# Kernel optimization log

Hardware: AMD Instinct MI355X
Metric: run time of the kernel (lower is better)

## Reference

```python
import jax, jax.numpy as jnp
import numpy as np

UNITS = 512
CONN = 512          # input feature dim (connections)
DEND_SIZE = 16
SEQL = CONN // DEND_SIZE  # 32 dendrite segments per unit
BATCH = 512


def _make_dendrites(units, conn, dsize, seed=0):
    # Per-unit random permutation of input indices, grouped into contiguous
    # dendrites of size dsize -> segment id in [0, seql) for every input index.
    rng = np.random.default_rng(seed)
    seql = conn // dsize
    seg = np.empty((units, conn), dtype=np.int32)
    for u in range(units):
        perm = rng.permutation(conn)
        for s in range(seql):
            seg[u, perm[dsize * s:dsize * (s + 1)]] = s
    return seg


def setup_inputs() -> dict:
    key = jax.random.key(0)
    k1, k2, k3, k4 = jax.random.split(key, 4)
    x = jax.random.normal(k1, (BATCH, CONN), dtype=jnp.float32)
    # weight_twice & not uniqueW -> per-unit scalar input weight, shape [1, units]
    kernel = jax.random.uniform(k2, (1, UNITS), dtype=jnp.float32, minval=5e-5, maxval=0.1)
    # per-(segment, unit) dendritic weight, shape [seql, units]
    dendriticW = jax.random.uniform(k3, (SEQL, UNITS), dtype=jnp.float32, minval=5e-5, maxval=0.1)
    bias = jax.random.normal(k4, (UNITS,), dtype=jnp.float32) * 0.05
    dendrites = jnp.asarray(_make_dendrites(UNITS, CONN, DEND_SIZE))  # [units, conn] int32
    return {"x": x, "kernel": kernel, "dendriticW": dendriticW,
            "bias": bias, "dendrites": dendrites}


def reference(x, kernel, dendriticW, bias, dendrites):
    # x: [batch, conn]; dendrites: [units, conn] segment ids in [0, SEQL)
    xT = x.T  # [conn, batch]
    # per-unit gather + unsorted_segment_sum over connections -> [units, seql, batch]
    segsum = jax.vmap(lambda seg: jax.ops.segment_sum(xT, seg, num_segments=SEQL))(dendrites)
    # weight_twice: per-unit scalar input weight (kernel broadcast over conn)
    segsum = segsum * kernel[0][:, None, None]
    # dendritic weighting + reduction over segments -> [batch, units]
    out = jnp.einsum('usb,su->bu', segsum, dendriticW) + bias
    return jax.nn.relu(out)
```

## Files before the change

### kernel.cpp

```cpp
#include <hip/hip_runtime.h>
#include <hip/hip_bf16.h>

#define UNITS 512
#define CONN  512
#define SEQL  32

typedef __hip_bfloat16 bf16;
typedef __attribute__((ext_vector_type(8))) short short8;
typedef __attribute__((ext_vector_type(4))) float floatx4;


union cv8 { bf16 h[8]; short8 v; };

__device__ __forceinline__ short8 cvt8(const float* p) {
    const float4 f0 = ((const float4*)p)[0];
    const float4 f1 = ((const float4*)p)[1];
    cv8 a;
    a.h[0] = __float2bfloat16(f0.x); a.h[1] = __float2bfloat16(f0.y);
    a.h[2] = __float2bfloat16(f0.z); a.h[3] = __float2bfloat16(f0.w);
    a.h[4] = __float2bfloat16(f1.x); a.h[5] = __float2bfloat16(f1.y);
    a.h[6] = __float2bfloat16(f1.z); a.h[7] = __float2bfloat16(f1.w);
    return a.v;
}

__global__ __launch_bounds__(256) void dendriter_fused_v2(
    const float* __restrict__ x,
    const float* __restrict__ kern,
    const float* __restrict__ dW,
    const float* __restrict__ bias,
    const int*   __restrict__ dend,
    float* __restrict__ out)
{
    __shared__ float  table[16][SEQL];
    __shared__ short8 wl[16][65];

    const int t  = threadIdx.x;
    const int ut = blockIdx.x * 16;
    const int bt = blockIdx.y * 64;

    const int lane = t & 63;
    const int wv   = t >> 6;
    const int m    = lane & 15;
    const int q    = lane >> 4;
    const int btw  = bt + wv * 16;
    const float* xrow = x + (size_t)(btw + m) * CONN + q * 8;
    short8 afr[16];
#pragma unroll
    for (int kb = 0; kb < 16; ++kb)
        afr[kb] = cvt8(xrow + kb * 32);

#pragma unroll
    for (int e = t; e < 16 * SEQL; e += 256) {
        const int seg = e >> 4, ul = e & 15;
        table[ul][seg] = kern[ut + ul] * dW[seg * UNITS + ut + ul];
    }
    __syncthreads();

    {
        const int ul  = t >> 4;
        const int cg0 = (t & 15) * 4;
        const int4* dp = (const int4*)(dend + (size_t)(ut + ul) * CONN + cg0 * 8);
#pragma unroll
        for (int j = 0; j < 4; ++j) {
            const int4 s0 = dp[2 * j];
            const int4 s1 = dp[2 * j + 1];
            const int segs[8] = {s0.x, s0.y, s0.z, s0.w, s1.x, s1.y, s1.z, s1.w};
            cv8 w;
#pragma unroll
            for (int i = 0; i < 8; ++i)
                w.h[i] = __float2bfloat16(table[ul][segs[i]]);
            const int cg = cg0 + j;
            wl[cg >> 2][ul | ((cg & 3) << 4)] = w.v;
        }
    }
    __syncthreads();

    floatx4 acc = {0.f, 0.f, 0.f, 0.f};
#pragma unroll
    for (int kb = 0; kb < 16; ++kb)
        acc = __builtin_amdgcn_mfma_f32_16x16x32_bf16(afr[kb], wl[kb][lane],
                                                      acc, 0, 0, 0);

    const float bu = bias[ut + m];
#pragma unroll
    for (int r = 0; r < 4; ++r) {
        float v = acc[r] + bu;
        v = v > 0.f ? v : 0.f;
        out[(size_t)(btw + q * 4 + r) * UNITS + ut + m] = v;
    }
}

extern "C" void kernel_launch(void* const* d_in, const int* in_sizes, int n_in,
                              void* d_out, int out_size, void* d_ws, size_t ws_size,
                              hipStream_t stream) {
    const float* x    = (const float*)d_in[0];
    const float* kern = (const float*)d_in[1];
    const float* dW   = (const float*)d_in[2];
    const float* bias = (const float*)d_in[3];
    const int*   dend = (const int*)  d_in[4];
    float* out = (float*)d_out;

    const int batch = in_sizes[0] / CONN;
    (void)d_ws; (void)ws_size;

    dendriter_fused_v2<<<dim3(UNITS / 16, batch / 64), 256, 0, stream>>>(
        x, kern, dW, bias, dend, out);
}
```

Baseline: 67.13 us.

## Split K dimension across waves with LDS reduction and shrink batch tile

Each block now covers 16 batch rows instead of 64, and its four waves split the 512-wide reduction into quarters, combining partial MFMA accumulators through shared memory. This launches four times as many blocks to raise parallelism and cuts per-thread register use for the x fragments. Dendrite index loads are also issued early into registers so they overlap the table build. In exchange the weight table is rebuilt four times as often across the grid, and an extra barrier plus LDS reduction is added.

```diff
diff --git a/kernel.cpp b/kernel.cpp
--- a/kernel.cpp
+++ b/kernel.cpp
@@ -23,7 +23,7 @@
     return a.v;
 }
 
-__global__ __launch_bounds__(256) void dendriter_fused_v2(
+__global__ __launch_bounds__(256) void dendriter_v3(
     const float* __restrict__ x,
     const float* __restrict__ kern,
     const float* __restrict__ dW,
@@ -31,62 +31,71 @@
     const int*   __restrict__ dend,
     float* __restrict__ out)
 {
-    __shared__ float  table[16][SEQL];
-    __shared__ short8 wl[16][65];
+    __shared__ float   table[16][SEQL];
+    __shared__ short8  wl[16][65];
+    __shared__ floatx4 red[3][64];
 
-    const int t  = threadIdx.x;
-    const int ut = blockIdx.x * 16;
-    const int bt = blockIdx.y * 64;
-
+    const int t    = threadIdx.x;
+    const int ut   = blockIdx.x * 16;
+    const int bt   = blockIdx.y * 16;
     const int lane = t & 63;
     const int wv   = t >> 6;
     const int m    = lane & 15;
     const int q    = lane >> 4;
-    const int btw  = bt + wv * 16;
-    const float* xrow = x + (size_t)(btw + m) * CONN + q * 8;
-    short8 afr[16];
+
+    const float* xrow = x + (size_t)(bt + m) * CONN + q * 8;
+    short8 afr[4];
 #pragma unroll
-    for (int kb = 0; kb < 16; ++kb)
-        afr[kb] = cvt8(xrow + kb * 32);
+    for (int j = 0; j < 4; ++j)
+        afr[j] = cvt8(xrow + (wv * 4 + j) * 32);
+
+    const int ul  = t >> 4;
+    const int cg0 = (t & 15) * 4;
+    const int4* dp = (const int4*)(dend + (size_t)(ut + ul) * CONN + cg0 * 8);
+    int4 sreg[8];
+#pragma unroll
+    for (int j = 0; j < 8; ++j) sreg[j] = dp[j];
 
 #pragma unroll
     for (int e = t; e < 16 * SEQL; e += 256) {
-        const int seg = e >> 4, ul = e & 15;
-        table[ul][seg] = kern[ut + ul] * dW[seg * UNITS + ut + ul];
+        const int seg = e >> 4, uu = e & 15;
+        table[uu][seg] = kern[ut + uu] * dW[seg * UNITS + ut + uu];
     }
     __syncthreads();
 
-    {
-        const int ul  = t >> 4;
-        const int cg0 = (t & 15) * 4;
-        const int4* dp = (const int4*)(dend + (size_t)(ut + ul) * CONN + cg0 * 8);
 #pragma unroll
-        for (int j = 0; j < 4; ++j) {
-            const int4 s0 = dp[2 * j];
-            const int4 s1 = dp[2 * j + 1];
-            const int segs[8] = {s0.x, s0.y, s0.z, s0.w, s1.x, s1.y, s1.z, s1.w};
-            cv8 w;
+    for (int j = 0; j < 4; ++j) {
+        const int4 s0 = sreg[2 * j];
+        const int4 s1 = sreg[2 * j + 1];
+        const int segs[8] = {s0.x, s0.y, s0.z, s0.w, s1.x, s1.y, s1.z, s1.w};
+        cv8 w;
 #pragma unroll
-            for (int i = 0; i < 8; ++i)
-                w.h[i] = __float2bfloat16(table[ul][segs[i]]);
-            const int cg = cg0 + j;
-            wl[cg >> 2][ul | ((cg & 3) << 4)] = w.v;
-        }
+        for (int i = 0; i < 8; ++i)
+            w.h[i] = __float2bfloat16(table[ul][segs[i]]);
+        const int cg = cg0 + j;
+        wl[cg >> 2][ul | ((cg & 3) << 4)] = w.v;
     }
     __syncthreads();
 
     floatx4 acc = {0.f, 0.f, 0.f, 0.f};
 #pragma unroll
-    for (int kb = 0; kb < 16; ++kb)
-        acc = __builtin_amdgcn_mfma_f32_16x16x32_bf16(afr[kb], wl[kb][lane],
-                                                      acc, 0, 0, 0);
+    for (int j = 0; j < 4; ++j)
+        acc = __builtin_amdgcn_mfma_f32_16x16x32_bf16(afr[j],
+                  wl[wv * 4 + j][lane], acc, 0, 0, 0);
 
-    const float bu = bias[ut + m];
+    if (wv) red[wv - 1][lane] = acc;
+    __syncthreads();
+    if (wv == 0) {
+        acc += red[0][lane];
+        acc += red[1][lane];
+        acc += red[2][lane];
+        const float bu = bias[ut + m];
 #pragma unroll
-    for (int r = 0; r < 4; ++r) {
-        float v = acc[r] + bu;
-        v = v > 0.f ? v : 0.f;
-        out[(size_t)(btw + q * 4 + r) * UNITS + ut + m] = v;
+        for (int r = 0; r < 4; ++r) {
+            float v = acc[r] + bu;
+            v = v > 0.f ? v : 0.f;
+            out[(size_t)(bt + q * 4 + r) * UNITS + ut + m] = v;
+        }
     }
 }
 
@@ -103,6 +112,6 @@
     const int batch = in_sizes[0] / CONN;
     (void)d_ws; (void)ws_size;
 
-    dendriter_fused_v2<<<dim3(UNITS / 16, batch / 64), 256, 0, stream>>>(
+    dendriter_v3<<<dim3(UNITS / 16, batch / 16), 256, 0, stream>>>(
         x, kern, dW, bias, dend, out);
 }
```

After: 70.04 us. 4.3% more time.
